# Kernel tuning notes

Measured on AMD Instinct MI355X. Metric: run time of the kernel, lower is better.

Reference implementation:

```python
import jax, jax.numpy as jnp
import numpy as np

C = 512
CQK = C // 8   # 64
CV = C // 4    # 128

def setup_inputs() -> dict:
    key = jax.random.key(0)
    ks = jax.random.split(key, 10)
    B, H, W = 4, 64, 64
    s = 1.0 / np.sqrt(C)
    x = jax.random.normal(ks[0], (B, C, H, W), dtype=jnp.float32)
    Wq = jax.random.normal(ks[1], (CQK, C), dtype=jnp.float32) * s
    bq = jnp.zeros((CQK,), jnp.float32)
    Wk = jax.random.normal(ks[2], (CQK, C), dtype=jnp.float32) * s
    bk = jnp.zeros((CQK,), jnp.float32)
    Wv = jax.random.normal(ks[3], (CV, C), dtype=jnp.float32) * s
    bv = jnp.zeros((CV,), jnp.float32)
    Wo = jax.random.normal(ks[4], (C, CV), dtype=jnp.float32) * (1.0 / np.sqrt(CV))
    bo = jnp.zeros((C,), jnp.float32)
    gamma = jnp.ones((1,), jnp.float32) * 0.5  # nonzero so out path matters
    return {"x": x, "Wq": Wq, "bq": bq, "Wk": Wk, "bk": bk,
            "Wv": Wv, "bv": bv, "Wo": Wo, "bo": bo, "gamma": gamma}

def reference(x, Wq, bq, Wk, bk, Wv, bv, Wo, bo, gamma):
    B, C_, H, W = x.shape
    N = H * W
    xf = x.reshape(B, C_, N)                       # [B,C,N]
    # 1x1 convs == channel matmuls
    q = jnp.einsum('oc,bcn->bno', Wq, xf) + bq     # [B,N,Cqk]
    k = jnp.einsum('oc,bcn->bon', Wk, xf) + bk[None, :, None]  # [B,Cqk,N]
    v = jnp.einsum('oc,bcn->bon', Wv, xf) + bv[None, :, None]  # [B,Cv,N]
    attn = jax.nn.softmax(jnp.einsum('bno,bom->bnm', q, k), axis=-1)  # [B,N,N]
    out = jnp.einsum('bom,bnm->bon', v, attn)      # [B,Cv,N]
    out = jnp.einsum('oc,bcn->bon', Wo, out) + bo[None, :, None]  # [B,C,N]
    out = out.reshape(B, C_, H, W)
    return x + gamma * out
```

## Files before the change

kernel.cpp:

```cpp
#include <hip/hip_runtime.h>
#include <cstdint>
#include <cstddef>

#define N_SP 4096
#define C_IN 512
#define C_QK 64
#define C_V  128
#define LOG2E 1.4426950408889634f

typedef unsigned short u16;
typedef __attribute__((ext_vector_type(8))) short bf16x8;
typedef __attribute__((ext_vector_type(4))) float f32x4;
typedef __attribute__((ext_vector_type(16))) float f32x16;

__device__ __forceinline__ u16 f2bf(float f) {
    union { float f; uint32_t u; } x; x.f = f;
    const uint32_t r = x.u + 0x7fffu + ((x.u >> 16) & 1u);
    return (u16)(r >> 16);
}
__device__ __forceinline__ float bf2f(u16 b) {
    union { uint32_t u; float f; } x; x.u = ((uint32_t)b) << 16;
    return x.f;
}

__device__ __forceinline__ void* swzPtr(void* base, int row, int colByte) {
    return (char*)base + row * 128 + (colByte ^ ((row & 7) << 4));
}

__device__ __forceinline__ void gl16(const u16* g, u16* l) {
    __builtin_amdgcn_global_load_lds(
        (const __attribute__((address_space(1))) void*)g,
        (__attribute__((address_space(3))) void*)l, 16, 0, 0);
}

__global__ __launch_bounds__(256) void transpose_kernel(
    const float* __restrict__ x, u16* __restrict__ xb)
{
    __shared__ u16 ts[64 * 64];
    const int t = threadIdx.x;
    const int b  = blockIdx.x & 3;
    const int cc = (blockIdx.x >> 2) & 7;
    const int nc = blockIdx.x >> 5;
    const int c0 = cc << 6, n0 = nc << 6;
    const float* xs = x + ((size_t)(b * C_IN + c0) << 12) + n0;
    for (int u = t; u < 1024; u += 256) {
        const int c = u >> 4, nq = (u & 15) << 2;
        const float4 v = *(const float4*)(xs + ((size_t)c << 12) + nq);
        ushort4 h;
        h.x = f2bf(v.x); h.y = f2bf(v.y); h.z = f2bf(v.z); h.w = f2bf(v.w);
        *(ushort4*)((char*)ts + c * 128 + ((nq << 1) ^ (((c >> 3) & 7) << 4))) = h;
    }
    __syncthreads();
    for (int u = t; u < 512; u += 256) {
        const int n = u >> 3, cg = u & 7;
        u16 pk[8];
        #pragma unroll
        for (int j = 0; j < 8; ++j) {
            const int c = (cg << 3) + j;
            pk[j] = *(const u16*)((char*)ts + c * 128 + ((n << 1) ^ (cg << 4)));
        }
        *(ushort4*)(xb + ((size_t)((b << 12) + n0 + n) << 9) + c0 + (cg << 3)) =
            *(ushort4*)&pk[0];
        *(ushort4*)(xb + ((size_t)((b << 12) + n0 + n) << 9) + c0 + (cg << 3) + 4) =
            *(ushort4*)&pk[4];
    }
}

__global__ __launch_bounds__(256) void qkv_kernel(
    const u16* __restrict__ xb,
    const float* __restrict__ Wq, const float* __restrict__ bq,
    const float* __restrict__ Wk, const float* __restrict__ bk,
    const float* __restrict__ Wv, const float* __restrict__ bv,
    u16* __restrict__ Qb, u16* __restrict__ Kb, u16* __restrict__ Vb)
{
    __shared__ u16 wt[64 * 64];
    __shared__ u16 xt[64 * 64];
    const int t = threadIdx.x;
    const int l = t & 63, w = t >> 6;
    const int lo = l & 15, hi = l >> 4;
    const int b  = blockIdx.x & 3;
    const int ot = (blockIdx.x >> 2) & 3;
    const int n0 = (blockIdx.x >> 4) << 6;
    const float* Wbase = (ot == 0) ? Wq : (ot == 1) ? Wk : (Wv + ((ot - 2) << 6) * C_IN);
    f32x4 acc[4];
    #pragma unroll
    for (int ti = 0; ti < 4; ++ti) acc[ti] = (f32x4){0.f, 0.f, 0.f, 0.f};

    for (int cc = 0; cc < 8; ++cc) {
        const int c0 = cc << 6;
        for (int u = t; u < 1024; u += 256) {
            const int i = u >> 4, c4 = (u & 15) << 2;
            const float4 v = *(const float4*)(Wbase + (size_t)i * C_IN + c0 + c4);
            ushort4 h;
            h.x = f2bf(v.x); h.y = f2bf(v.y); h.z = f2bf(v.z); h.w = f2bf(v.w);
            *(ushort4*)swzPtr(wt, i, c4 << 1) = h;
        }
        for (int u = t; u < 512; u += 256) {
            const int i = u >> 3, cb = (u & 7) << 4;
            *(uint4*)swzPtr(xt, i, cb) =
                *(const uint4*)(xb + ((size_t)((b << 12) + n0 + i) << 9) + c0 + (cb >> 1));
        }
        __syncthreads();
        if (ot < 2) {
            const bf16x8 af0 = *(const bf16x8*)swzPtr(xt, (w << 4) + lo, hi << 4);
            const bf16x8 af1 = *(const bf16x8*)swzPtr(xt, (w << 4) + lo, 64 + (hi << 4));
            #pragma unroll
            for (int ti = 0; ti < 4; ++ti) {
                const bf16x8 bf0 = *(const bf16x8*)swzPtr(wt, (ti << 4) + lo, hi << 4);
                const bf16x8 bf1 = *(const bf16x8*)swzPtr(wt, (ti << 4) + lo, 64 + (hi << 4));
                acc[ti] = __builtin_amdgcn_mfma_f32_16x16x32_bf16(af0, bf0, acc[ti], 0, 0, 0);
                acc[ti] = __builtin_amdgcn_mfma_f32_16x16x32_bf16(af1, bf1, acc[ti], 0, 0, 0);
            }
        } else {
            const bf16x8 af0 = *(const bf16x8*)swzPtr(wt, (w << 4) + lo, hi << 4);
            const bf16x8 af1 = *(const bf16x8*)swzPtr(wt, (w << 4) + lo, 64 + (hi << 4));
            #pragma unroll
            for (int ti = 0; ti < 4; ++ti) {
                const bf16x8 bf0 = *(const bf16x8*)swzPtr(xt, (ti << 4) + lo, hi << 4);
                const bf16x8 bf1 = *(const bf16x8*)swzPtr(xt, (ti << 4) + lo, 64 + (hi << 4));
                acc[ti] = __builtin_amdgcn_mfma_f32_16x16x32_bf16(af0, bf0, acc[ti], 0, 0, 0);
                acc[ti] = __builtin_amdgcn_mfma_f32_16x16x32_bf16(af1, bf1, acc[ti], 0, 0, 0);
            }
        }
        __syncthreads();
    }
    if (ot < 2) {
        const float* bias_base = (ot == 0) ? bq : bk;
        u16* dst = (ot == 0) ? Qb : Kb;
        const float sc = (ot == 0) ? LOG2E : 1.0f;
        #pragma unroll
        for (int ti = 0; ti < 4; ++ti) {
            const float bias = bias_base[(ti << 4) + lo];
            #pragma unroll
            for (int r = 0; r < 4; ++r) {
                const int nrow = (w << 4) + (hi << 2) + r;
                dst[((size_t)((b << 12) + n0 + nrow) << 6) + (ti << 4) + lo] =
                    f2bf((acc[ti][r] + bias) * sc);
            }
        }
    } else {
        #pragma unroll
        for (int r = 0; r < 4; ++r) {
            const int cv = ((ot - 2) << 6) + (w << 4) + (hi << 2) + r;
            const float bias = bv[cv];
            #pragma unroll
            for (int ti = 0; ti < 4; ++ti)
                Vb[((size_t)(b * C_V + cv) << 12) + n0 + (ti << 4) + lo] =
                    f2bf(acc[ti][r] + bias);
        }
    }
}

__global__ __launch_bounds__(256, 2) void attn_kernel(
    const u16* __restrict__ Qb, const u16* __restrict__ Kb,
    const u16* __restrict__ Vb, u16* __restrict__ po,
    float* __restrict__ pm, float* __restrict__ pl)
{
    __shared__ u16 ksm[2][64 * 64];
    __shared__ u16 vsm[2][128 * 64];
    const int t = threadIdx.x;
    const int l = t & 63, w = t >> 6;
    const int l31 = l & 31, h = l >> 5;
    const int b = blockIdx.x & 3;
    const int s = (blockIdx.x >> 2) & 3;
    const int qc = blockIdx.x >> 4;
    const int n0 = qc << 7;
    const int colOff = ((l & 7) ^ (l >> 3)) << 3;
    const u16* kbase = Kb + ((size_t)b << 18);
    const u16* vbase = Vb + ((size_t)(b * C_V) << 12);
    const int m0base = s << 10;

    const u16* qrow_p = Qb + ((size_t)((b << 12) + n0 + (w << 5) + l31) << 6) + (h << 3);
    bf16x8 qf[4];
    #pragma unroll
    for (int ks = 0; ks < 4; ++ks) qf[ks] = *(const bf16x8*)(qrow_p + (ks << 4));

    #pragma unroll
    for (int i = 0; i < 2; ++i) {
        const int kr = (w << 4) + (i << 3);
        gl16(kbase + ((size_t)(m0base + kr + (l >> 3)) << 6) + colOff, &ksm[0][kr << 6]);
    }
    #pragma unroll
    for (int i = 0; i < 4; ++i) {
        const int cv = (w << 5) + (i << 3);
        gl16(vbase + ((size_t)(cv + (l >> 3)) << 12) + m0base + colOff, &vsm[0][cv << 6]);
    }
    float m_run = -1e30f, lsum = 0.f;
    f32x16 oacc[4];
    #pragma unroll
    for (int tj = 0; tj < 4; ++tj)
        #pragma unroll
        for (int i = 0; i < 16; ++i) oacc[tj][i] = 0.f;
    asm volatile("s_waitcnt vmcnt(0)" ::: "memory");
    __syncthreads();

    int cur = 0;
    for (int kt = 0; kt < 16; ++kt) {
        if (kt < 15) {
            const int m1 = m0base + ((kt + 1) << 6);
            #pragma unroll
            for (int i = 0; i < 2; ++i) {
                const int kr = (w << 4) + (i << 3);
                gl16(kbase + ((size_t)(m1 + kr + (l >> 3)) << 6) + colOff,
                     &ksm[cur ^ 1][kr << 6]);
            }
            #pragma unroll
            for (int i = 0; i < 4; ++i) {
                const int cv = (w << 5) + (i << 3);
                gl16(vbase + ((size_t)(cv + (l >> 3)) << 12) + m1 + colOff,
                     &vsm[cur ^ 1][cv << 6]);
            }
        }
        f32x16 sa0, sa1;
        #pragma unroll
        for (int i = 0; i < 16; ++i) { sa0[i] = 0.f; sa1[i] = 0.f; }
        #pragma unroll
        for (int ks = 0; ks < 4; ++ks) {
            const bf16x8 k0 = *(const bf16x8*)swzPtr(ksm[cur], l31,      (h << 4) + (ks << 5));
            const bf16x8 k1 = *(const bf16x8*)swzPtr(ksm[cur], 32 + l31, (h << 4) + (ks << 5));
            sa0 = __builtin_amdgcn_mfma_f32_32x32x16_bf16(k0, qf[ks], sa0, 0, 0, 0);
            sa1 = __builtin_amdgcn_mfma_f32_32x32x16_bf16(k1, qf[ks], sa1, 0, 0, 0);
        }
        float mx[8];
        #pragma unroll
        for (int i = 0; i < 8; ++i)
            mx[i] = fmaxf(fmaxf(sa0[i], sa0[i + 8]), fmaxf(sa1[i], sa1[i + 8]));
        #pragma unroll
        for (int i = 0; i < 4; ++i) mx[i] = fmaxf(mx[i], mx[i + 4]);
        mx[0] = fmaxf(fmaxf(mx[0], mx[1]), fmaxf(mx[2], mx[3]));
        const float pmax = fmaxf(mx[0], __shfl_xor(mx[0], 32));
        if (!__all(pmax <= m_run + 8.0f)) {
            const float nm = fmaxf(m_run, pmax);
            const float al = exp2f(m_run - nm);
            m_run = nm;
            #pragma unroll
            for (int tj = 0; tj < 4; ++tj)
                #pragma unroll
                for (int i = 0; i < 16; ++i) oacc[tj][i] *= al;
            lsum *= al;
        }
        float p0[16], p1[16];
        #pragma unroll
        for (int i = 0; i < 16; ++i) {
            p0[i] = exp2f(sa0[i] - m_run);
            p1[i] = exp2f(sa1[i] - m_run);
        }
        float sm8[8];
        #pragma unroll
        for (int i = 0; i < 8; ++i) sm8[i] = (p0[i] + p0[i + 8]) + (p1[i] + p1[i + 8]);
        #pragma unroll
        for (int i = 0; i < 4; ++i) sm8[i] += sm8[i + 4];
        float ps = (sm8[0] + sm8[1]) + (sm8[2] + sm8[3]);
        ps += __shfl_xor(ps, 32);
        lsum += ps;
        uint32_t P2[2][4][2];
        #pragma unroll
        for (int g = 0; g < 4; ++g)
            #pragma unroll
            for (int pr = 0; pr < 2; ++pr) {
                asm("v_cvt_pk_bf16_f32 %0, %1, %2"
                    : "=v"(P2[0][g][pr]) : "v"(p0[4 * g + 2 * pr]), "v"(p0[4 * g + 2 * pr + 1]));
                asm("v_cvt_pk_bf16_f32 %0, %1, %2"
                    : "=v"(P2[1][g][pr]) : "v"(p1[4 * g + 2 * pr]), "v"(p1[4 * g + 2 * pr + 1]));
            }
        bf16x8 pf[4];
        #pragma unroll
        for (int ks = 0; ks < 4; ++ks) {
            const int iE = ks << 1, iO = iE + 1;
            uint32_t fr[4];
            #pragma unroll
            for (int pr = 0; pr < 2; ++pr) {
                const uint32_t X = P2[iE >> 2][iE & 3][pr];
                const uint32_t Y = P2[iO >> 2][iO & 3][pr];
                const uint32_t Xs = (uint32_t)__shfl_xor((int)X, 32);
                const uint32_t Ys = (uint32_t)__shfl_xor((int)Y, 32);
                fr[pr]     = h ? Ys : X;
                fr[2 + pr] = h ? Y  : Xs;
            }
            pf[ks] = *(bf16x8*)fr;
        }
        #pragma unroll
        for (int tj = 0; tj < 4; ++tj)
            #pragma unroll
            for (int ks = 0; ks < 4; ++ks) {
                const bf16x8 vf =
                    *(const bf16x8*)swzPtr(vsm[cur], (tj << 5) + l31, (h << 4) + (ks << 5));
                oacc[tj] = __builtin_amdgcn_mfma_f32_32x32x16_bf16(vf, pf[ks], oacc[tj], 0, 0, 0);
            }
        asm volatile("s_waitcnt vmcnt(0)" ::: "memory");
        __syncthreads();
        cur ^= 1;
    }
    u16* pod = po + ((size_t)blockIdx.x << 14);
    #pragma unroll
    for (int tj = 0; tj < 4; ++tj)
        #pragma unroll
        for (int r = 0; r < 16; ++r) {
            const int cv = (tj << 5) + (r & 3) + ((r >> 2) << 3) + (h << 2);
            pod[(cv << 7) + (w << 5) + l31] = f2bf(oacc[tj][r]);
        }
    if (h == 0) {
        pm[(blockIdx.x << 7) + (w << 5) + l31] = m_run;
        pl[(blockIdx.x << 7) + (w << 5) + l31] = lsum;
    }
}

__global__ __launch_bounds__(256) void combine_kernel(
    const u16* __restrict__ po, const float* __restrict__ pm,
    const float* __restrict__ pl, u16* __restrict__ Ob)
{
    __shared__ float fs[4][128];
    __shared__ float invl[128];
    __shared__ float tr[64][132];
    const int t = threadIdx.x;
    const int b = blockIdx.x & 3;
    const int qc = blockIdx.x >> 2;
    int slot[4];
    #pragma unroll
    for (int s = 0; s < 4; ++s) slot[s] = b + (s << 2) + (qc << 4);
    if (t < 128) {
        const float m0 = pm[(slot[0] << 7) + t], m1 = pm[(slot[1] << 7) + t];
        const float m2 = pm[(slot[2] << 7) + t], m3 = pm[(slot[3] << 7) + t];
        const float mg = fmaxf(fmaxf(m0, m1), fmaxf(m2, m3));
        const float f0 = exp2f(m0 - mg), f1 = exp2f(m1 - mg);
        const float f2 = exp2f(m2 - mg), f3 = exp2f(m3 - mg);
        const float lg = pl[(slot[0] << 7) + t] * f0 + pl[(slot[1] << 7) + t] * f1 +
                         pl[(slot[2] << 7) + t] * f2 + pl[(slot[3] << 7) + t] * f3;
        fs[0][t] = f0; fs[1][t] = f1; fs[2][t] = f2; fs[3][t] = f3;
        invl[t] = 1.0f / lg;
    }
    __syncthreads();
    #pragma unroll
    for (int qh = 0; qh < 2; ++qh) {
        for (int u = t; u < 2048; u += 256) {
            const int cv = u >> 4, q4 = (u & 15) << 2;
            const int q = (qh << 6) + q4;
            float a0 = 0.f, a1 = 0.f, a2 = 0.f, a3 = 0.f;
            #pragma unroll
            for (int s = 0; s < 4; ++s) {
                const ushort4 hv =
                    *(const ushort4*)(po + ((size_t)slot[s] << 14) + (cv << 7) + q);
                a0 += bf2f(hv.x) * fs[s][q];
                a1 += bf2f(hv.y) * fs[s][q + 1];
                a2 += bf2f(hv.z) * fs[s][q + 2];
                a3 += bf2f(hv.w) * fs[s][q + 3];
            }
            tr[q4 + 0][cv] = a0 * invl[q];
            tr[q4 + 1][cv] = a1 * invl[q + 1];
            tr[q4 + 2][cv] = a2 * invl[q + 2];
            tr[q4 + 3][cv] = a3 * invl[q + 3];
        }
        __syncthreads();
        for (int u = t; u < 2048; u += 256) {
            const int q = u >> 5, c4 = (u & 31) << 2;
            const float4 v = *(const float4*)&tr[q][c4];
            ushort4 o;
            o.x = f2bf(v.x); o.y = f2bf(v.y); o.z = f2bf(v.z); o.w = f2bf(v.w);
            const int n = (qc << 7) + (qh << 6) + q;
            *(ushort4*)(Ob + ((size_t)((b << 12) + n) << 7) + c4) = o;
        }
        __syncthreads();
    }
}

__global__ __launch_bounds__(256) void proj_kernel(
    const u16* __restrict__ Ob, const float* __restrict__ Wo,
    const float* __restrict__ bo, const float* __restrict__ x,
    const float* __restrict__ gamma_p, float* __restrict__ out)
{
    __shared__ union {
        struct { u16 wl0[64 * 64]; u16 wl1[64 * 64]; u16 ob0[64 * 64]; u16 ob1[64 * 64]; } s;
        float tr[64 * 64];
    } sm;
    const int t = threadIdx.x;
    const int l = t & 63, w = t >> 6;
    const int lo = l & 15, hi = l >> 4;
    const int b  = blockIdx.x & 3;
    const int co0 = ((blockIdx.x >> 2) & 7) << 6;
    const int n0  = (blockIdx.x >> 5) << 6;
    for (int u = t; u < 2048; u += 256) {
        const int i = u >> 5, c4 = (u & 31) << 2;
        const float4 v = *(const float4*)(Wo + (size_t)(co0 + i) * C_V + c4);
        ushort4 h;
        h.x = f2bf(v.x); h.y = f2bf(v.y); h.z = f2bf(v.z); h.w = f2bf(v.w);
        *(ushort4*)swzPtr((c4 < 64) ? sm.s.wl0 : sm.s.wl1, i, (c4 & 63) << 1) = h;
    }
    for (int u = t; u < 1024; u += 256) {
        const int i = u >> 4, cb = (u & 15) << 4;
        *(uint4*)swzPtr((cb < 128) ? sm.s.ob0 : sm.s.ob1, i, cb & 127) =
            *(const uint4*)(Ob + ((size_t)((b << 12) + n0 + i) << 7) + (cb >> 1));
    }
    __syncthreads();
    const int arow = (w << 4) + lo;
    const bf16x8 af00 = *(const bf16x8*)swzPtr(sm.s.wl0, arow, hi << 4);
    const bf16x8 af01 = *(const bf16x8*)swzPtr(sm.s.wl0, arow, 64 + (hi << 4));
    const bf16x8 af10 = *(const bf16x8*)swzPtr(sm.s.wl1, arow, hi << 4);
    const bf16x8 af11 = *(const bf16x8*)swzPtr(sm.s.wl1, arow, 64 + (hi << 4));
    f32x4 acc[4];
    #pragma unroll
    for (int ti = 0; ti < 4; ++ti) {
        const int brow = (ti << 4) + lo;
        f32x4 z = (f32x4){0.f, 0.f, 0.f, 0.f};
        z = __builtin_amdgcn_mfma_f32_16x16x32_bf16(af00, *(const bf16x8*)swzPtr(sm.s.ob0, brow, hi << 4), z, 0, 0, 0);
        z = __builtin_amdgcn_mfma_f32_16x16x32_bf16(af01, *(const bf16x8*)swzPtr(sm.s.ob0, brow, 64 + (hi << 4)), z, 0, 0, 0);
        z = __builtin_amdgcn_mfma_f32_16x16x32_bf16(af10, *(const bf16x8*)swzPtr(sm.s.ob1, brow, hi << 4), z, 0, 0, 0);
        acc[ti] = __builtin_amdgcn_mfma_f32_16x16x32_bf16(af11, *(const bf16x8*)swzPtr(sm.s.ob1, brow, 64 + (hi << 4)), z, 0, 0, 0);
    }
    __syncthreads();
    #pragma unroll
    for (int ti = 0; ti < 4; ++ti)
        #pragma unroll
        for (int r = 0; r < 4; ++r) {
            const int co = (w << 4) + (hi << 2) + r;
            const int n  = (ti << 4) + lo;
            sm.tr[(co << 6) + (n ^ (((co >> 2) & 3) << 2))] = acc[ti][r];
        }
    __syncthreads();
    const float g = gamma_p[0];
    for (int u = t; u < 1024; u += 256) {
        const int co = u >> 4, n4 = (u & 15) << 2;
        const float4 av = *(const float4*)&sm.tr[(co << 6) + (n4 ^ (((co >> 2) & 3) << 2))];
        const int o = co0 + co;
        const size_t off = ((size_t)(b * C_IN + o) << 12) + n0 + n4;
        const float4 xv = *(const float4*)(x + off);
        const float bias = bo[o];
        float4 rs;
        rs.x = xv.x + g * (av.x + bias);
        rs.y = xv.y + g * (av.y + bias);
        rs.z = xv.z + g * (av.z + bias);
        rs.w = xv.w + g * (av.w + bias);
        *(float4*)(out + off) = rs;
    }
}

extern "C" void kernel_launch(void* const* d_in, const int* in_sizes, int n_in,
                              void* d_out, int out_size, void* d_ws, size_t ws_size,
                              hipStream_t stream) {
    (void)in_sizes; (void)n_in; (void)out_size; (void)ws_size;
    const float* x  = (const float*)d_in[0];
    const float* Wq = (const float*)d_in[1];
    const float* bq = (const float*)d_in[2];
    const float* Wk = (const float*)d_in[3];
    const float* bk = (const float*)d_in[4];
    const float* Wv = (const float*)d_in[5];
    const float* bv = (const float*)d_in[6];
    const float* Wo = (const float*)d_in[7];
    const float* bo = (const float*)d_in[8];
    const float* gm = (const float*)d_in[9];
    float* out = (float*)d_out;
    u16* xb = (u16*)d_ws;
    u16* po = (u16*)d_ws;
    u16* Qb = xb + (size_t)8 * 1024 * 1024;
    u16* Kb = Qb + (size_t)4 * N_SP * C_QK;
    u16* Vb = Kb + (size_t)4 * N_SP * C_QK;
    float* pm = (float*)(Vb + (size_t)4 * C_V * N_SP);
    float* pl = pm + 512 * 128;
    u16* Ob = (u16*)(pl + 512 * 128);
    transpose_kernel<<<2048, 256, 0, stream>>>(x, xb);
    qkv_kernel<<<1024, 256, 0, stream>>>(xb, Wq, bq, Wk, bk, Wv, bv, Qb, Kb, Vb);
    attn_kernel<<<512, 256, 0, stream>>>(Qb, Kb, Vb, po, pm, pl);
    combine_kernel<<<128, 256, 0, stream>>>(po, pm, pl, Ob);
    proj_kernel<<<2048, 256, 0, stream>>>(Ob, Wo, bo, x, gm, out);
}
```

Baseline: 113.6 us.

## Software-pipeline attention loop: overlap next QK^T with softmax/PV, triple-buffer V

Restructures the flash-attention inner loop so the S=QK^T MFMAs for tile t+1 are issued alongside the softmax and PV of tile t. Prefetch runs two tiles ahead, with V triple-buffered and K double-buffered, and partial vmcnt waits replace full drains. It also adds s_setprio around the MFMA blocks, merges two cross-half shuffles into one, and defers the lsum cross-lane reduction to the end. The aim is to hide load latency and let MFMA overlap the exp/VALU work, at the cost of more LDS and registers, which may reduce occupancy at 2 blocks per CU.

```diff
diff --git a/kernel.cpp b/kernel.cpp
--- a/kernel.cpp
+++ b/kernel.cpp
@@ -23,7 +23,7 @@
     return x.f;
 }
 
-__device__ __forceinline__ void* swzPtr(void* base, int row, int colByte) {
+__device__ __forceinline__ void* swzPtr(const void* base, int row, int colByte) {
     return (char*)base + row * 128 + (colByte ^ ((row & 7) << 4));
 }
 
@@ -151,13 +151,135 @@
     }
 }
 
+
+__device__ __forceinline__ void stageK(const u16* kbase, int m, u16* kdst,
+                                       int w, int l, int colOff) {
+    #pragma unroll
+    for (int i = 0; i < 2; ++i) {
+        const int kr = (w << 4) + (i << 3);
+        gl16(kbase + ((size_t)(m + kr + (l >> 3)) << 6) + colOff, kdst + (kr << 6));
+    }
+}
+__device__ __forceinline__ void stageV(const u16* vbase, int m, u16* vdst,
+                                       int w, int l, int colOff) {
+    #pragma unroll
+    for (int i = 0; i < 4; ++i) {
+        const int cv = (w << 5) + (i << 3);
+        gl16(vbase + ((size_t)(cv + (l >> 3)) << 12) + m + colOff, vdst + (cv << 6));
+    }
+}
+__device__ __forceinline__ void computeS(const u16* kbuf, const bf16x8* qf,
+                                         int l31, int h, f32x16& s0, f32x16& s1) {
+    #pragma unroll
+    for (int i = 0; i < 16; ++i) { s0[i] = 0.f; s1[i] = 0.f; }
+    __builtin_amdgcn_s_setprio(1);
+    #pragma unroll
+    for (int ks = 0; ks < 4; ++ks) {
+        const bf16x8 k0 = *(const bf16x8*)swzPtr(kbuf, l31,      (h << 4) + (ks << 5));
+        const bf16x8 k1 = *(const bf16x8*)swzPtr(kbuf, 32 + l31, (h << 4) + (ks << 5));
+        s0 = __builtin_amdgcn_mfma_f32_32x32x16_bf16(k0, qf[ks], s0, 0, 0, 0);
+        s1 = __builtin_amdgcn_mfma_f32_32x32x16_bf16(k1, qf[ks], s1, 0, 0, 0);
+    }
+    __builtin_amdgcn_s_setprio(0);
+}
+__device__ __forceinline__ void softmaxPV(f32x16& sa0, f32x16& sa1, const u16* vbuf,
+                                          float& m_run, float& lsum,
+                                          f32x16 (&oacc)[4], int l31, int h) {
+    float mx[8];
+    #pragma unroll
+    for (int i = 0; i < 8; ++i)
+        mx[i] = fmaxf(fmaxf(sa0[i], sa0[i + 8]), fmaxf(sa1[i], sa1[i + 8]));
+    #pragma unroll
+    for (int i = 0; i < 4; ++i) mx[i] = fmaxf(mx[i], mx[i + 4]);
+    mx[0] = fmaxf(fmaxf(mx[0], mx[1]), fmaxf(mx[2], mx[3]));
+    const float pmax = fmaxf(mx[0], __shfl_xor(mx[0], 32));
+    if (!__all(pmax <= m_run + 8.0f)) {
+        const float nm = fmaxf(m_run, pmax);
+        const float al = exp2f(m_run - nm);
+        m_run = nm;
+        #pragma unroll
+        for (int tj = 0; tj < 4; ++tj)
+            #pragma unroll
+            for (int i = 0; i < 16; ++i) oacc[tj][i] *= al;
+        lsum *= al;
+    }
+    float p0[16], p1[16];
+    #pragma unroll
+    for (int i = 0; i < 16; ++i) {
+        p0[i] = exp2f(sa0[i] - m_run);
+        p1[i] = exp2f(sa1[i] - m_run);
+    }
+    float sm8[8];
+    #pragma unroll
+    for (int i = 0; i < 8; ++i) sm8[i] = (p0[i] + p0[i + 8]) + (p1[i] + p1[i + 8]);
+    #pragma unroll
+    for (int i = 0; i < 4; ++i) sm8[i] += sm8[i + 4];
+    lsum += (sm8[0] + sm8[1]) + (sm8[2] + sm8[3]);
+    uint32_t P2[2][4][2];
+    #pragma unroll
+    for (int g = 0; g < 4; ++g)
+        #pragma unroll
+        for (int pr = 0; pr < 2; ++pr) {
+            asm("v_cvt_pk_bf16_f32 %0, %1, %2"
+                : "=v"(P2[0][g][pr]) : "v"(p0[4 * g + 2 * pr]), "v"(p0[4 * g + 2 * pr + 1]));
+            asm("v_cvt_pk_bf16_f32 %0, %1, %2"
+                : "=v"(P2[1][g][pr]) : "v"(p1[4 * g + 2 * pr]), "v"(p1[4 * g + 2 * pr + 1]));
+        }
+    bf16x8 pf[4];
+    #pragma unroll
+    for (int ks = 0; ks < 4; ++ks) {
+        const int iE = ks << 1, iO = iE + 1;
+        uint32_t fr[4];
+        #pragma unroll
+        for (int pr = 0; pr < 2; ++pr) {
+            const uint32_t X = P2[iE >> 2][iE & 3][pr];
+            const uint32_t Y = P2[iO >> 2][iO & 3][pr];
+            const uint32_t send = h ? X : Y;
+            const uint32_t recv = (uint32_t)__shfl_xor((int)send, 32);
+            fr[pr]     = h ? recv : X;
+            fr[2 + pr] = h ? Y : recv;
+        }
+        pf[ks] = *(bf16x8*)fr;
+    }
+    __builtin_amdgcn_s_setprio(1);
+    #pragma unroll
+    for (int tj = 0; tj < 4; ++tj)
+        #pragma unroll
+        for (int ks = 0; ks < 4; ++ks) {
+            const bf16x8 vf =
+                *(const bf16x8*)swzPtr(vbuf, (tj << 5) + l31, (h << 4) + (ks << 5));
+            oacc[tj] = __builtin_amdgcn_mfma_f32_32x32x16_bf16(vf, pf[ks], oacc[tj], 0, 0, 0);
+        }
+    __builtin_amdgcn_s_setprio(0);
+}
+
+template<bool ISSUE>
+__device__ __forceinline__ void attn_iter(
+    int t, const u16* kbase, const u16* vbase, int m0base,
+    u16* k_read, u16* k_write, u16* v_cur, u16* v_fly,
+    const bf16x8* qf, f32x16& c0, f32x16& c1, f32x16& n0v, f32x16& n1v,
+    float& m_run, float& lsum, f32x16 (&oacc)[4],
+    int w, int l, int l31, int h, int colOff)
+{
+    asm volatile("s_waitcnt vmcnt(4)" ::: "memory");
+    __builtin_amdgcn_s_barrier();
+    __builtin_amdgcn_sched_barrier(0);
+    if (ISSUE) {
+        const int m2 = m0base + ((t + 2) << 6);
+        stageK(kbase, m2, k_write, w, l, colOff);
+        stageV(vbase, m2, v_fly, w, l, colOff);
+    }
+    computeS(k_read, qf, l31, h, n0v, n1v);
+    softmaxPV(c0, c1, v_cur, m_run, lsum, oacc, l31, h);
+}
+
 __global__ __launch_bounds__(256, 2) void attn_kernel(
     const u16* __restrict__ Qb, const u16* __restrict__ Kb,
     const u16* __restrict__ Vb, u16* __restrict__ po,
     float* __restrict__ pm, float* __restrict__ pl)
 {
     __shared__ u16 ksm[2][64 * 64];
-    __shared__ u16 vsm[2][128 * 64];
+    __shared__ u16 vsm[3][128 * 64];
     const int t = threadIdx.x;
     const int l = t & 63, w = t >> 6;
     const int l31 = l & 31, h = l >> 5;
@@ -175,122 +297,46 @@
     #pragma unroll
     for (int ks = 0; ks < 4; ++ks) qf[ks] = *(const bf16x8*)(qrow_p + (ks << 4));
 
-    #pragma unroll
-    for (int i = 0; i < 2; ++i) {
-        const int kr = (w << 4) + (i << 3);
-        gl16(kbase + ((size_t)(m0base + kr + (l >> 3)) << 6) + colOff, &ksm[0][kr << 6]);
-    }
-    #pragma unroll
-    for (int i = 0; i < 4; ++i) {
-        const int cv = (w << 5) + (i << 3);
-        gl16(vbase + ((size_t)(cv + (l >> 3)) << 12) + m0base + colOff, &vsm[0][cv << 6]);
-    }
+    stageK(kbase, m0base,      ksm[0], w, l, colOff);
+    stageV(vbase, m0base,      vsm[0], w, l, colOff);
+    stageK(kbase, m0base + 64, ksm[1], w, l, colOff);
+    stageV(vbase, m0base + 64, vsm[1], w, l, colOff);
+
     float m_run = -1e30f, lsum = 0.f;
     f32x16 oacc[4];
     #pragma unroll
     for (int tj = 0; tj < 4; ++tj)
         #pragma unroll
         for (int i = 0; i < 16; ++i) oacc[tj][i] = 0.f;
+
+    asm volatile("s_waitcnt vmcnt(10)" ::: "memory");
+    __builtin_amdgcn_s_barrier();
+    __builtin_amdgcn_sched_barrier(0);
+
+    f32x16 A0, A1, B0, B1;
+    computeS(ksm[0], qf, l31, h, A0, A1);
+
+    u16 *kr_ = ksm[1], *kw_ = ksm[0];
+    u16 *vc = vsm[0], *vn = vsm[1], *vf = vsm[2];
+    for (int tt = 0; tt < 14; tt += 2) {
+        attn_iter<true>(tt, kbase, vbase, m0base, kr_, kw_, vc, vf,
+                        qf, A0, A1, B0, B1, m_run, lsum, oacc, w, l, l31, h, colOff);
+        { u16* tk = kr_; kr_ = kw_; kw_ = tk; }
+        { u16* tv = vc; vc = vn; vn = vf; vf = tv; }
+        attn_iter<true>(tt + 1, kbase, vbase, m0base, kr_, kw_, vc, vf,
+                        qf, B0, B1, A0, A1, m_run, lsum, oacc, w, l, l31, h, colOff);
+        { u16* tk = kr_; kr_ = kw_; kw_ = tk; }
+        { u16* tv = vc; vc = vn; vn = vf; vf = tv; }
+    }
+    attn_iter<false>(14, kbase, vbase, m0base, kr_, kw_, vc, vf,
+                     qf, A0, A1, B0, B1, m_run, lsum, oacc, w, l, l31, h, colOff);
+    { u16* tv = vc; vc = vn; vn = vf; vf = tv; }
     asm volatile("s_waitcnt vmcnt(0)" ::: "memory");
-    __syncthreads();
-
-    int cur = 0;
-    for (int kt = 0; kt < 16; ++kt) {
-        if (kt < 15) {
-            const int m1 = m0base + ((kt + 1) << 6);
-            #pragma unroll
-            for (int i = 0; i < 2; ++i) {
-                const int kr = (w << 4) + (i << 3);
-                gl16(kbase + ((size_t)(m1 + kr + (l >> 3)) << 6) + colOff,
-                     &ksm[cur ^ 1][kr << 6]);
-            }
-            #pragma unroll
-            for (int i = 0; i < 4; ++i) {
-                const int cv = (w << 5) + (i << 3);
-                gl16(vbase + ((size_t)(cv + (l >> 3)) << 12) + m1 + colOff,
-                     &vsm[cur ^ 1][cv << 6]);
-            }
-        }
-        f32x16 sa0, sa1;
-        #pragma unroll
-        for (int i = 0; i < 16; ++i) { sa0[i] = 0.f; sa1[i] = 0.f; }
-        #pragma unroll
-        for (int ks = 0; ks < 4; ++ks) {
-            const bf16x8 k0 = *(const bf16x8*)swzPtr(ksm[cur], l31,      (h << 4) + (ks << 5));
-            const bf16x8 k1 = *(const bf16x8*)swzPtr(ksm[cur], 32 + l31, (h << 4) + (ks << 5));
-            sa0 = __builtin_amdgcn_mfma_f32_32x32x16_bf16(k0, qf[ks], sa0, 0, 0, 0);
-            sa1 = __builtin_amdgcn_mfma_f32_32x32x16_bf16(k1, qf[ks], sa1, 0, 0, 0);
-        }
-        float mx[8];
-        #pragma unroll
-        for (int i = 0; i < 8; ++i)
-            mx[i] = fmaxf(fmaxf(sa0[i], sa0[i + 8]), fmaxf(sa1[i], sa1[i + 8]));
-        #pragma unroll
-        for (int i = 0; i < 4; ++i) mx[i] = fmaxf(mx[i], mx[i + 4]);
-        mx[0] = fmaxf(fmaxf(mx[0], mx[1]), fmaxf(mx[2], mx[3]));
-        const float pmax = fmaxf(mx[0], __shfl_xor(mx[0], 32));
-        if (!__all(pmax <= m_run + 8.0f)) {
-            const float nm = fmaxf(m_run, pmax);
-            const float al = exp2f(m_run - nm);
-            m_run = nm;
-            #pragma unroll
-            for (int tj = 0; tj < 4; ++tj)
-                #pragma unroll
-                for (int i = 0; i < 16; ++i) oacc[tj][i] *= al;
-            lsum *= al;
-        }
-        float p0[16], p1[16];
-        #pragma unroll
-        for (int i = 0; i < 16; ++i) {
-            p0[i] = exp2f(sa0[i] - m_run);
-            p1[i] = exp2f(sa1[i] - m_run);
-        }
-        float sm8[8];
-        #pragma unroll
-        for (int i = 0; i < 8; ++i) sm8[i] = (p0[i] + p0[i + 8]) + (p1[i] + p1[i + 8]);
-        #pragma unroll
-        for (int i = 0; i < 4; ++i) sm8[i] += sm8[i + 4];
-        float ps = (sm8[0] + sm8[1]) + (sm8[2] + sm8[3]);
-        ps += __shfl_xor(ps, 32);
-        lsum += ps;
-        uint32_t P2[2][4][2];
-        #pragma unroll
-        for (int g = 0; g < 4; ++g)
-            #pragma unroll
-            for (int pr = 0; pr < 2; ++pr) {
-                asm("v_cvt_pk_bf16_f32 %0, %1, %2"
-                    : "=v"(P2[0][g][pr]) : "v"(p0[4 * g + 2 * pr]), "v"(p0[4 * g + 2 * pr + 1]));
-                asm("v_cvt_pk_bf16_f32 %0, %1, %2"
-                    : "=v"(P2[1][g][pr]) : "v"(p1[4 * g + 2 * pr]), "v"(p1[4 * g + 2 * pr + 1]));
-            }
-        bf16x8 pf[4];
-        #pragma unroll
-        for (int ks = 0; ks < 4; ++ks) {
-            const int iE = ks << 1, iO = iE + 1;
-            uint32_t fr[4];
-            #pragma unroll
-            for (int pr = 0; pr < 2; ++pr) {
-                const uint32_t X = P2[iE >> 2][iE & 3][pr];
-                const uint32_t Y = P2[iO >> 2][iO & 3][pr];
-                const uint32_t Xs = (uint32_t)__shfl_xor((int)X, 32);
-                const uint32_t Ys = (uint32_t)__shfl_xor((int)Y, 32);
-                fr[pr]     = h ? Ys : X;
-                fr[2 + pr] = h ? Y  : Xs;
-            }
-            pf[ks] = *(bf16x8*)fr;
-        }
-        #pragma unroll
-        for (int tj = 0; tj < 4; ++tj)
-            #pragma unroll
-            for (int ks = 0; ks < 4; ++ks) {
-                const bf16x8 vf =
-                    *(const bf16x8*)swzPtr(vsm[cur], (tj << 5) + l31, (h << 4) + (ks << 5));
-                oacc[tj] = __builtin_amdgcn_mfma_f32_32x32x16_bf16(vf, pf[ks], oacc[tj], 0, 0, 0);
-            }
-        asm volatile("s_waitcnt vmcnt(0)" ::: "memory");
-        __syncthreads();
-        cur ^= 1;
-    }
+    __builtin_amdgcn_s_barrier();
+    __builtin_amdgcn_sched_barrier(0);
+    softmaxPV(B0, B1, vc, m_run, lsum, oacc, l31, h);
+
+    lsum += __shfl_xor(lsum, 32);
     u16* pod = po + ((size_t)blockIdx.x << 14);
     #pragma unroll
     for (int tj = 0; tj < 4; ++tj)
```

New measurement: 113.1 us. About the same (-0.4%).
